# Performance work log

Measured on AMD Instinct MI355X. Metric: run time of the kernel, lower is better.

Reference implementation:

```python
import jax, jax.numpy as jnp
import numpy as np

DIM = 384
DSTATE = 16
DTRANK = 24  # ceil(384/16)
DCONV = 3
F = 3  # fixed segment factor from rearrange 'b (f t) c'


def setup_inputs() -> dict:
    key = jax.random.key(0)
    ks = jax.random.split(key, 8)
    d_in = DIM // 2
    x = jax.random.normal(ks[0], (4, 6144, DIM), dtype=jnp.float32)
    in_proj_w = jax.random.normal(ks[1], (DIM, DIM), dtype=jnp.float32) * 0.05
    in_proj_b = jnp.zeros((DIM,), jnp.float32)
    conv_w = jax.random.normal(ks[2], (d_in, 2, DCONV), dtype=jnp.float32) * 0.3
    conv_b = jnp.zeros((d_in,), jnp.float32)
    A = jnp.tile(jnp.arange(1, DSTATE + 1, dtype=jnp.float32)[None, :], (d_in, 1))
    A_log = jnp.log(A)
    Ab_log = jnp.log(A)
    D = jnp.ones((d_in,), jnp.float32)
    x_proj_w = jax.random.normal(ks[3], (DTRANK + 2 * DSTATE, d_in), dtype=jnp.float32) * 0.05
    dt_init_std = DTRANK ** (-0.5)
    dt_proj_w = jax.random.uniform(ks[4], (d_in, DTRANK), minval=-dt_init_std, maxval=dt_init_std, dtype=jnp.float32)
    dt = jnp.exp(jax.random.uniform(ks[5], (d_in,), dtype=jnp.float32) * (np.log(0.1) - np.log(0.001)) + np.log(0.001))
    dt = jnp.clip(dt, 1e-4)
    dt_proj_b = dt + jnp.log(-jnp.expm1(-dt))
    out_proj_w = jax.random.normal(ks[6], (DIM, DIM), dtype=jnp.float32) * 0.05
    out_proj_b = jnp.zeros((DIM,), jnp.float32)
    return dict(x=x, in_proj_w=in_proj_w, in_proj_b=in_proj_b, conv_w=conv_w, conv_b=conv_b,
                A_log=A_log, Ab_log=Ab_log, D=D, x_proj_w=x_proj_w, dt_proj_w=dt_proj_w,
                dt_proj_b=dt_proj_b, out_proj_w=out_proj_w, out_proj_b=out_proj_b)


def _ssm(u, Amat, x_proj_w, dt_proj_w, dt_proj_b, Dvec):
    # u: (b, d, l) selective scan (no z-gating; z handled outside by concat)
    x_dbl = jnp.einsum('rd,bdl->brl', x_proj_w, u)
    dt = x_dbl[:, :DTRANK]                      # (b, r, l)
    Bm = x_dbl[:, DTRANK:DTRANK + DSTATE]       # (b, n, l)
    Cm = x_dbl[:, DTRANK + DSTATE:]             # (b, n, l)
    delta = jax.nn.softplus(jnp.einsum('dr,brl->bdl', dt_proj_w, dt) + dt_proj_b[None, :, None])
    dA = jnp.exp(jnp.einsum('bdl,dn->lbdn', delta, Amat))      # (l, b, d, n)
    dBu = jnp.einsum('bdl,bnl->lbdn', delta * u, Bm)           # (l, b, d, n)
    Ct = jnp.transpose(Cm, (2, 0, 1))                          # (l, b, n)
    h0 = jnp.zeros(u.shape[:2] + (DSTATE,), u.dtype)

    def step(h, inp):
        dA_t, dBu_t, C_t = inp
        h = dA_t * h + dBu_t
        return h, jnp.einsum('bdn,bn->bd', h, C_t)

    _, ys = jax.lax.scan(step, h0, (dA, dBu, Ct))
    return jnp.transpose(ys, (1, 2, 0)) + u * Dvec[None, :, None]


def reference(x, in_proj_w, in_proj_b, conv_w, conv_b, A_log, Ab_log, D,
              x_proj_w, dt_proj_w, dt_proj_b, out_proj_w, out_proj_b):
    b, seqlen, dim = x.shape
    t = seqlen // F
    xp = (x @ in_proj_w.T + in_proj_b).reshape(b * F, t, dim)
    xp = jnp.transpose(xp, (0, 2, 1))  # (bf, dim, t)
    xc = jax.lax.conv_general_dilated(xp, conv_w, (1,), 'SAME',
                                      dimension_numbers=('NCH', 'OIH', 'NCH'),
                                      feature_group_count=dim // 2)
    xc = jax.nn.silu(xc + conv_b[None, :, None])  # (bf, dim//2, t)
    z = xc
    A = -jnp.exp(A_log)
    Ab = -jnp.exp(Ab_log)
    fwd = _ssm(xc, A, x_proj_w, dt_proj_w, dt_proj_b, D)
    bwd = jnp.flip(_ssm(jnp.flip(xc, -1), Ab, x_proj_w, dt_proj_w, dt_proj_b, D), -1)
    y = jnp.concatenate([fwd + bwd, z], axis=1)   # (bf, dim, t)
    y = jnp.transpose(y, (0, 2, 1))
    out = y @ out_proj_w.T + out_proj_b
    return out.reshape(b, seqlen, dim)
```

## Files before the change

### kernel.cpp

```cpp
#include <hip/hip_runtime.h>
#include <hip/hip_bf16.h>
#include <math.h>

#define NSQ   12
#define LQ    2048
#define DIMQ  384
#define DIQ   192
#define RKQ   24
#define NCHK  16
#define CLEN  128

#define BM 128
#define BN 64
#define BK 64

typedef unsigned short u16;
typedef __attribute__((ext_vector_type(8))) short s16x8;
typedef __attribute__((ext_vector_type(4))) float f32x4;
typedef __attribute__((ext_vector_type(4))) unsigned short u16x4;
typedef __attribute__((ext_vector_type(8))) unsigned short u16x8;

__device__ __forceinline__ float siluf(float x) {
  return x / (1.0f + __expf(-x));
}
__device__ __forceinline__ float softplusf(float x) {
  return (x > 20.0f) ? x : log1pf(expf(x));
}
__device__ __forceinline__ u16 f2bf(float f) {
  unsigned int u = __float_as_uint(f);
  u += 0x7FFFu + ((u >> 16) & 1u);
  return (u16)(u >> 16);
}

union F4 { float4 v; float a[4]; };

template<int CTRL>
__device__ __forceinline__ float dpp_add(float x) {
  union { float f; int i; } u, r;
  u.f = x;
  r.i = __builtin_amdgcn_update_dpp(0, u.i, CTRL, 0xF, 0xF, true);
  return x + r.f;
}

__global__ void k_prep(const float* __restrict__ xpw, const float* __restrict__ dtw,
                       const float* __restrict__ inw, const float* __restrict__ outw,
                       float* __restrict__ xpw_t, float* __restrict__ dtw_t,
                       u16* __restrict__ winb, u16* __restrict__ woutb) {
  int t = threadIdx.x + blockIdx.x * blockDim.x;
  int stride = blockDim.x * gridDim.x;
  for (int i = t; i < DIQ * 56; i += stride) {
    int d = i / 56, r = i % 56;
    xpw_t[i] = xpw[r * DIQ + d];
  }
  for (int i = t; i < RKQ * DIQ; i += stride) {
    int r = i / DIQ, d = i % DIQ;
    dtw_t[i] = dtw[d * RKQ + r];
  }
  for (int i = t; i < DIMQ * DIMQ; i += stride) {
    winb[i]  = f2bf(inw[i]);
    woutb[i] = f2bf(outw[i]);
  }
}

__launch_bounds__(256)
__global__ void k_inproj(const float* __restrict__ x, const u16* __restrict__ wbf,
                         const float* __restrict__ bias, float* __restrict__ xp_t) {
  __shared__ __align__(16) char smem[33792];
  u16 (*As)[72] = (u16(*)[72])smem;
  u16 (*Bs)[72] = (u16(*)[72])(smem + 18432);
  const int t = threadIdx.x;
  const int m0 = blockIdx.x * BM;
  const int n0 = blockIdx.y * BN;
  const int lane = t & 63, wid = t >> 6;
  const int wm = wid >> 1, wn = wid & 1;
  const int lr = lane & 15, lg = lane >> 4;
  f32x4 acc[4][2];
#pragma unroll
  for (int i = 0; i < 4; ++i)
#pragma unroll
    for (int j = 0; j < 2; ++j) acc[i][j] = (f32x4){0.f, 0.f, 0.f, 0.f};

  for (int k0 = 0; k0 < 384; k0 += BK) {
    float4 a_ld[8];
#pragma unroll
    for (int i = 0; i < 8; ++i) {
      const int idx = t + i * 256;
      const int row = idx >> 4, kq = (idx & 15) * 4;
      a_ld[i] = *(const float4*)&x[(size_t)(m0 + row) * 384 + k0 + kq];
    }
    u16x8 b_ld[2];
#pragma unroll
    for (int i = 0; i < 2; ++i) {
      const int idx = t + i * 256;
      const int n = idx >> 3, kq = (idx & 7) * 8;
      b_ld[i] = *(const u16x8*)&wbf[(size_t)(n0 + n) * 384 + k0 + kq];
    }
    __syncthreads();
#pragma unroll
    for (int i = 0; i < 8; ++i) {
      const int idx = t + i * 256;
      const int row = idx >> 4, kq = (idx & 15) * 4;
      u16x4 p;
      p.x = f2bf(a_ld[i].x); p.y = f2bf(a_ld[i].y);
      p.z = f2bf(a_ld[i].z); p.w = f2bf(a_ld[i].w);
      *(u16x4*)&As[row][kq] = p;
    }
#pragma unroll
    for (int i = 0; i < 2; ++i) {
      const int idx = t + i * 256;
      const int n = idx >> 3, kq = (idx & 7) * 8;
      *(u16x8*)&Bs[n][kq] = b_ld[i];
    }
    __syncthreads();
#pragma unroll
    for (int kh = 0; kh < BK; kh += 32) {
      s16x8 af[4], bf[2];
#pragma unroll
      for (int mi = 0; mi < 4; ++mi)
        af[mi] = *(const s16x8*)&As[wm * 64 + mi * 16 + lr][kh + lg * 8];
#pragma unroll
      for (int ni = 0; ni < 2; ++ni)
        bf[ni] = *(const s16x8*)&Bs[wn * 32 + ni * 16 + lr][kh + lg * 8];
#pragma unroll
      for (int mi = 0; mi < 4; ++mi)
#pragma unroll
        for (int ni = 0; ni < 2; ++ni)
          acc[mi][ni] = __builtin_amdgcn_mfma_f32_16x16x32_bf16(af[mi], bf[ni], acc[mi][ni], 0, 0, 0);
    }
    __syncthreads();
  }
  float (*T)[132] = (float(*)[132])smem;
#pragma unroll
  for (int mi = 0; mi < 4; ++mi)
#pragma unroll
    for (int ni = 0; ni < 2; ++ni) {
      const int c_loc = wn * 32 + ni * 16 + lr;
      const int m_loc = wm * 64 + mi * 16 + lg * 4;
      *(f32x4*)&T[c_loc][m_loc] = acc[mi][ni];
    }
  __syncthreads();
  const int s = m0 >> 11, p0 = m0 & 2047;
#pragma unroll
  for (int i = 0; i < 8; ++i) {
    const int idx = t + i * 256;
    const int c = idx >> 5, pq = (idx & 31) * 4;
    float4 v = *(const float4*)&T[c][pq];
    const float bv = bias[n0 + c];
    v.x += bv; v.y += bv; v.z += bv; v.w += bv;
    *(float4*)&xp_t[((size_t)s * 384 + n0 + c) * 2048 + p0 + pq] = v;
  }
}

__global__ void k_conv(const float* __restrict__ xp_t, const float* __restrict__ cw,
                       const float* __restrict__ cb, float* __restrict__ xc) {
  const int idx = blockIdx.x * 256 + threadIdx.x;
  const int p = idx & 2047;
  const int sd = idx >> 11;
  const int d = sd % DIQ, s = sd / DIQ;
  const float* r0 = &xp_t[((size_t)s * 384 + 2 * d) * 2048];
  const float* r1 = r0 + 2048;
  const float w00 = cw[d * 6 + 0], w01 = cw[d * 6 + 1], w02 = cw[d * 6 + 2];
  const float w10 = cw[d * 6 + 3], w11 = cw[d * 6 + 4], w12 = cw[d * 6 + 5];
  float acc = cb[d];
  if (p > 0)    acc += w00 * r0[p - 1] + w10 * r1[p - 1];
  acc += w01 * r0[p] + w11 * r1[p];
  if (p < 2047) acc += w02 * r0[p + 1] + w12 * r1[p + 1];
  xc[idx] = siluf(acc);
}

__launch_bounds__(256)
__global__ void k_xproj(const float* __restrict__ xc, const float* __restrict__ xpw_t,
                        const float* __restrict__ dtw_t, const float* __restrict__ dtb,
                        float* __restrict__ delta, float* __restrict__ bc) {
  __shared__ float As[16][68];
  __shared__ float Bs[16][64];
  __shared__ float xd[24][68];
  __shared__ float Dtw[24][192];
  const int t = threadIdx.x;
  const int m0 = blockIdx.x * 64;
  const int s = m0 >> 11, l0 = m0 & 2047;
  for (int i = t; i < 24 * 192; i += 256) Dtw[i / 192][i % 192] = dtw_t[i];
  const int tx = t & 15, ty = t >> 4;
  const int lk = t >> 4, mq = t & 15;
  float acc[4][4];
#pragma unroll
  for (int i = 0; i < 4; ++i)
#pragma unroll
    for (int j = 0; j < 4; ++j) acc[i][j] = 0.0f;

  for (int k0 = 0; k0 < 192; k0 += 16) {
    const float4 a = *(const float4*)&xc[((size_t)s * 192 + k0 + lk) * 2048 + l0 + mq * 4];
    float4 b;
    if (mq < 14) b = *(const float4*)&xpw_t[(size_t)(k0 + lk) * 56 + mq * 4];
    else         b = make_float4(0.f, 0.f, 0.f, 0.f);
    __syncthreads();
    *(float4*)&As[lk][mq * 4] = a;
    *(float4*)&Bs[lk][mq * 4] = b;
    __syncthreads();
#pragma unroll
    for (int k = 0; k < 16; ++k) {
      const float4 av = *(const float4*)&As[k][tx * 4];
      const float4 bv = *(const float4*)&Bs[k][ty * 4];
      const float a4[4] = {av.x, av.y, av.z, av.w};
      const float b4[4] = {bv.x, bv.y, bv.z, bv.w};
#pragma unroll
      for (int i = 0; i < 4; ++i)
#pragma unroll
        for (int j = 0; j < 4; ++j) acc[i][j] = fmaf(a4[i], b4[j], acc[i][j]);
    }
  }
  const int nbase = ty * 4;
  if (nbase < 24) {
#pragma unroll
    for (int j = 0; j < 4; ++j)
#pragma unroll
      for (int i = 0; i < 4; ++i) xd[nbase + j][tx * 4 + i] = acc[i][j];
  } else if (nbase < 56) {
#pragma unroll
    for (int i = 0; i < 4; ++i) {
      float4 v; v.x = acc[i][0]; v.y = acc[i][1]; v.z = acc[i][2]; v.w = acc[i][3];
      *(float4*)&bc[(size_t)(m0 + tx * 4 + i) * 32 + (nbase - 24)] = v;
    }
  }
  __syncthreads();
#pragma unroll
  for (int dc = 0; dc < 3; ++dc) {
    float a2[4][4];
#pragma unroll
    for (int i = 0; i < 4; ++i)
#pragma unroll
      for (int j = 0; j < 4; ++j) a2[i][j] = 0.0f;
    const int d0 = dc * 64 + ty * 4;
#pragma unroll
    for (int r = 0; r < 24; ++r) {
      const float4 av = *(const float4*)&xd[r][tx * 4];
      const float4 bv = *(const float4*)&Dtw[r][d0];
      const float a4[4] = {av.x, av.y, av.z, av.w};
      const float b4[4] = {bv.x, bv.y, bv.z, bv.w};
#pragma unroll
      for (int i = 0; i < 4; ++i)
#pragma unroll
        for (int j = 0; j < 4; ++j) a2[i][j] = fmaf(a4[i], b4[j], a2[i][j]);
    }
#pragma unroll
    for (int j = 0; j < 4; ++j) {
      const int d = d0 + j;
      const float bb = dtb[d];
      float4 v;
      v.x = softplusf(a2[0][j] + bb);
      v.y = softplusf(a2[1][j] + bb);
      v.z = softplusf(a2[2][j] + bb);
      v.w = softplusf(a2[3][j] + bb);
      *(float4*)&delta[((size_t)s * 192 + d) * 2048 + l0 + tx * 4] = v;
    }
  }
}

template<int DIR>
__launch_bounds__(256)
__global__ void k_scanA(const float* __restrict__ delta, const float* __restrict__ xc,
                        const float* __restrict__ bc, const float* __restrict__ A_log,
                        const float* __restrict__ Ab_log,
                        float* __restrict__ G, float* __restrict__ hc) {
  __shared__ float dch[16][132];
  __shared__ float uch[16][132];
  __shared__ float bsn[16][132];
  const int t = threadIdx.x;
  const int dl = t >> 4, n = t & 15;
  const int dg = blockIdx.x;
  const int s  = blockIdx.y;
  const int tc = blockIdx.z;
  const int d = dg * 16 + dl;
  const int base_l = DIR ? (LQ - CLEN * (tc + 1)) : (CLEN * tc);
  const float a = -__expf((DIR ? Ab_log : A_log)[d * 16 + n]);

  const size_t rb = ((size_t)s * 192 + dg * 16) * 2048 + base_l;
#pragma unroll
  for (int it = 0; it < 2; ++it) {
    const int i = t + it * 256;
    const int row = i >> 5, c4 = (i & 31) * 4;
    *(float4*)&dch[row][c4] = *(const float4*)&delta[rb + (size_t)row * 2048 + c4];
    *(float4*)&uch[row][c4] = *(const float4*)&xc[rb + (size_t)row * 2048 + c4];
  }
  const size_t bb = ((size_t)s * 2048 + base_l) * 32;
#pragma unroll
  for (int it = 0; it < 2; ++it) {
    const int i = t + it * 256;
    const int l = i >> 2, nq = (i & 3) * 4;
    F4 v; v.v = *(const float4*)&bc[bb + (size_t)l * 32 + nq];
#pragma unroll
    for (int k = 0; k < 4; ++k) bsn[nq + k][l] = v.a[k];
  }
  __syncthreads();
  float h = 0.0f, S = 0.0f;
#pragma unroll 4
  for (int qx = 0; qx < 32; ++qx) {
    const int q = DIR ? (31 - qx) : qx;
    const int lq = q * 4;
    F4 d4, u4, b4;
    d4.v = *(const float4*)&dch[dl][lq];
    u4.v = *(const float4*)&uch[dl][lq];
    b4.v = *(const float4*)&bsn[n][lq];
#pragma unroll
    for (int jj = 0; jj < 4; ++jj) {
      const int j = DIR ? (3 - jj) : jj;
      const float dlt = d4.a[j];
      const float dA = __expf(a * dlt);
      h = fmaf(dA, h, dlt * u4.a[j] * b4.a[j]);
      S += dlt;
    }
  }
  const size_t idx = (((size_t)(s * 2 + DIR) * NCHK + tc) * 192 + d) * 16 + n;
  G[idx] = __expf(a * S);
  hc[idx] = h;
}

__global__ void k_scanB(const float* __restrict__ G, float* __restrict__ hc) {
  const int gid = blockIdx.x * 256 + threadIdx.x;
  const int sd2 = gid / 3072;
  const int dn = gid % 3072;
  float h = 0.0f;
#pragma unroll
  for (int tc = 0; tc < NCHK; ++tc) {
    const size_t idx = ((size_t)sd2 * NCHK + tc) * 3072 + dn;
    const float g = G[idx];
    const float he = hc[idx];
    hc[idx] = h;
    h = fmaf(g, h, he);
  }
}

template<int DIR>
__launch_bounds__(256)
__global__ void k_scanC(const float* __restrict__ delta, const float* __restrict__ xc,
                        const float* __restrict__ bc, const float* __restrict__ A_log,
                        const float* __restrict__ Ab_log, const float* __restrict__ hc,
                        float* __restrict__ yf, float* __restrict__ yb) {
  __shared__ float dch[16][132];
  __shared__ float uch[16][132];
  __shared__ float bsn[16][132];
  __shared__ float csn[16][132];
  const int t = threadIdx.x;
  const int dl = t >> 4, n = t & 15;
  const int dg = blockIdx.x;
  const int s  = blockIdx.y;
  const int tc = blockIdx.z;
  const int d = dg * 16 + dl;
  const int base_l = DIR ? (LQ - CLEN * (tc + 1)) : (CLEN * tc);
  const float a = -__expf((DIR ? Ab_log : A_log)[d * 16 + n]);

  const size_t rb = ((size_t)s * 192 + dg * 16) * 2048 + base_l;
#pragma unroll
  for (int it = 0; it < 2; ++it) {
    const int i = t + it * 256;
    const int row = i >> 5, c4 = (i & 31) * 4;
    *(float4*)&dch[row][c4] = *(const float4*)&delta[rb + (size_t)row * 2048 + c4];
    *(float4*)&uch[row][c4] = *(const float4*)&xc[rb + (size_t)row * 2048 + c4];
  }
  const size_t bb = ((size_t)s * 2048 + base_l) * 32;
#pragma unroll
  for (int it = 0; it < 4; ++it) {
    const int i = t + it * 256;
    const int l = i >> 3, cq = (i & 7) * 4;
    F4 v; v.v = *(const float4*)&bc[bb + (size_t)l * 32 + cq];
    if (cq < 16) {
#pragma unroll
      for (int k = 0; k < 4; ++k) bsn[cq + k][l] = v.a[k];
    } else {
#pragma unroll
      for (int k = 0; k < 4; ++k) csn[cq - 16 + k][l] = v.a[k];
    }
  }
  const size_t idx = (((size_t)(s * 2 + DIR) * NCHK + tc) * 192 + d) * 16 + n;
  float h = hc[idx];
  __syncthreads();
  float* yrow = &(DIR ? yb : yf)[((size_t)s * 192 + d) * 2048 + base_l];
#pragma unroll 2
  for (int ww = 0; ww < 8; ++ww) {
    const int w = DIR ? (7 - ww) : ww;
    float ykeep = 0.0f;
#pragma unroll
    for (int qq = 0; qq < 4; ++qq) {
      const int q = DIR ? (3 - qq) : qq;
      const int lq = w * 16 + q * 4;
      F4 d4, u4, b4, c4;
      d4.v = *(const float4*)&dch[dl][lq];
      u4.v = *(const float4*)&uch[dl][lq];
      b4.v = *(const float4*)&bsn[n][lq];
      c4.v = *(const float4*)&csn[n][lq];
#pragma unroll
      for (int jj = 0; jj < 4; ++jj) {
        const int j = DIR ? (3 - jj) : jj;
        const float dlt = d4.a[j];
        const float dA = __expf(a * dlt);
        h = fmaf(dA, h, dlt * u4.a[j] * b4.a[j]);
        float yv = h * c4.a[j];
        yv = dpp_add<0x128>(yv);
        yv = dpp_add<0x124>(yv);
        yv = dpp_add<0x122>(yv);
        yv = dpp_add<0x121>(yv);
        ykeep = (q * 4 + j == n) ? yv : ykeep;
      }
    }
    yrow[w * 16 + n] = ykeep;
  }
}

#define SWC(l) (((l >> 2) & 7) << 3)
__launch_bounds__(256)
__global__ void k_combine(const float* __restrict__ yf, const float* __restrict__ yb,
                          const float* __restrict__ xc, const float* __restrict__ Dvec,
                          u16* __restrict__ Abuf) {
  __shared__ u16 T[64][72];
  const int t = threadIdx.x;
  const int cg = blockIdx.x;
  const int s  = blockIdx.y;
  const int l0 = blockIdx.z * 64;
  const int c0 = (cg < 3 ? cg : cg - 3) * 64;
#pragma unroll
  for (int i = 0; i < 4; ++i) {
    const int idx = t + i * 256;
    const int cr = idx >> 4, lq = (idx & 15) * 4;
    const size_t off = ((size_t)s * 192 + c0 + cr) * 2048 + l0 + lq;
    F4 v;
    if (cg < 3) {
      F4 f, g, u;
      f.v = *(const float4*)&yf[off];
      g.v = *(const float4*)&yb[off];
      u.v = *(const float4*)&xc[off];
      const float dv2 = 2.0f * Dvec[c0 + cr];
#pragma unroll
      for (int j = 0; j < 4; ++j) v.a[j] = f.a[j] + g.a[j] + dv2 * u.a[j];
    } else {
      v.v = *(const float4*)&xc[off];
    }
#pragma unroll
    for (int j = 0; j < 4; ++j) {
      const int l = lq + j;
      T[l][cr ^ SWC(l)] = f2bf(v.a[j]);
    }
  }
  __syncthreads();
  const int ccol = (cg < 3) ? cg * 64 : 192 + (cg - 3) * 64;
#pragma unroll
  for (int i = 0; i < 2; ++i) {
    const int idx = t + i * 256;
    const int l = idx >> 3, cq = (idx & 7) * 8;
    const u16x8 v = *(const u16x8*)&T[l][cq ^ SWC(l)];
    *(u16x8*)&Abuf[((size_t)s * 2048 + l0 + l) * 384 + ccol + cq] = v;
  }
}

__launch_bounds__(256)
__global__ void k_outproj(const u16* __restrict__ Abuf, const u16* __restrict__ wbf,
                          const float* __restrict__ bias, float* __restrict__ out) {
  __shared__ __align__(16) char smem[34816];
  u16 (*As)[72] = (u16(*)[72])smem;
  u16 (*Bs)[72] = (u16(*)[72])(smem + 18432);
  const int t = threadIdx.x;
  const int m0 = blockIdx.x * BM;
  const int n0 = blockIdx.y * BN;
  const int lane = t & 63, wid = t >> 6;
  const int wm = wid >> 1, wn = wid & 1;
  const int lr = lane & 15, lg = lane >> 4;
  f32x4 acc[4][2];
#pragma unroll
  for (int i = 0; i < 4; ++i)
#pragma unroll
    for (int j = 0; j < 2; ++j) acc[i][j] = (f32x4){0.f, 0.f, 0.f, 0.f};

  for (int k0 = 0; k0 < 384; k0 += BK) {
    u16x8 a_ld[4];
#pragma unroll
    for (int i = 0; i < 4; ++i) {
      const int idx = t + i * 256;
      const int row = idx >> 3, kq = (idx & 7) * 8;
      a_ld[i] = *(const u16x8*)&Abuf[(size_t)(m0 + row) * 384 + k0 + kq];
    }
    u16x8 b_ld[2];
#pragma unroll
    for (int i = 0; i < 2; ++i) {
      const int idx = t + i * 256;
      const int n = idx >> 3, kq = (idx & 7) * 8;
      b_ld[i] = *(const u16x8*)&wbf[(size_t)(n0 + n) * 384 + k0 + kq];
    }
    __syncthreads();
#pragma unroll
    for (int i = 0; i < 4; ++i) {
      const int idx = t + i * 256;
      const int row = idx >> 3, kq = (idx & 7) * 8;
      *(u16x8*)&As[row][kq] = a_ld[i];
    }
#pragma unroll
    for (int i = 0; i < 2; ++i) {
      const int idx = t + i * 256;
      const int n = idx >> 3, kq = (idx & 7) * 8;
      *(u16x8*)&Bs[n][kq] = b_ld[i];
    }
    __syncthreads();
#pragma unroll
    for (int kh = 0; kh < BK; kh += 32) {
      s16x8 af[4], bf[2];
#pragma unroll
      for (int mi = 0; mi < 4; ++mi)
        af[mi] = *(const s16x8*)&As[wm * 64 + mi * 16 + lr][kh + lg * 8];
#pragma unroll
      for (int ni = 0; ni < 2; ++ni)
        bf[ni] = *(const s16x8*)&Bs[wn * 32 + ni * 16 + lr][kh + lg * 8];
#pragma unroll
      for (int mi = 0; mi < 4; ++mi)
#pragma unroll
        for (int ni = 0; ni < 2; ++ni)
          acc[mi][ni] = __builtin_amdgcn_mfma_f32_16x16x32_bf16(af[mi], bf[ni], acc[mi][ni], 0, 0, 0);
    }
    __syncthreads();
  }
  float (*T)[68] = (float(*)[68])smem;
#pragma unroll
  for (int mi = 0; mi < 4; ++mi)
#pragma unroll
    for (int ni = 0; ni < 2; ++ni) {
      const int c_loc = wn * 32 + ni * 16 + lr;
      const int m_loc = wm * 64 + mi * 16 + lg * 4;
#pragma unroll
      for (int r = 0; r < 4; ++r) T[m_loc + r][c_loc] = acc[mi][ni][r];
    }
  __syncthreads();
#pragma unroll
  for (int i = 0; i < 8; ++i) {
    const int idx = t + i * 256;
    const int m = idx >> 4, cq = (idx & 15) * 4;
    float4 v = *(const float4*)&T[m][cq];
    const float4 bb = *(const float4*)&bias[n0 + cq];
    v.x += bb.x; v.y += bb.y; v.z += bb.z; v.w += bb.w;
    *(float4*)&out[(size_t)(m0 + m) * 384 + n0 + cq] = v;
  }
}

extern "C" void kernel_launch(void* const* d_in, const int* in_sizes, int n_in,
                              void* d_out, int out_size, void* d_ws, size_t ws_size,
                              hipStream_t stream) {
  const float* x     = (const float*)d_in[0];
  const float* inw   = (const float*)d_in[1];
  const float* inb   = (const float*)d_in[2];
  const float* convw = (const float*)d_in[3];
  const float* convb = (const float*)d_in[4];
  const float* alog  = (const float*)d_in[5];
  const float* ablog = (const float*)d_in[6];
  const float* Dv    = (const float*)d_in[7];
  const float* xpw   = (const float*)d_in[8];
  const float* dtw   = (const float*)d_in[9];
  const float* dtb   = (const float*)d_in[10];
  const float* outw  = (const float*)d_in[11];
  const float* outb  = (const float*)d_in[12];
  float* out = (float*)d_out;

  float* ws = (float*)d_ws;
  float* xp_t  = ws;
  float* xc    = xp_t + 9437184;
  float* delta = xc + 4718592;
  float* bc    = delta + 4718592;
  float* xpw_t = bc + 786432;
  float* dtw_t = xpw_t + 10752;
  float* G     = dtw_t + 4608;
  float* hc    = G + 1179648;
  u16*   winb  = (u16*)(hc + 1179648);
  u16*   woutb = winb + 147456;
  float* yf = xp_t;
  float* yb = xp_t + 4718592;
  u16*   Abuf = (u16*)delta;

  hipLaunchKernelGGL(k_prep,      dim3(96),         dim3(256), 0, stream, xpw, dtw, inw, outw, xpw_t, dtw_t, winb, woutb);
  hipLaunchKernelGGL(k_inproj,    dim3(192, 6),     dim3(256), 0, stream, x, winb, inb, xp_t);
  hipLaunchKernelGGL(k_conv,      dim3(18432),      dim3(256), 0, stream, xp_t, convw, convb, xc);
  hipLaunchKernelGGL(k_xproj,     dim3(384),        dim3(256), 0, stream, xc, xpw_t, dtw_t, dtb, delta, bc);
  hipLaunchKernelGGL((k_scanA<0>),dim3(12, 12, 16), dim3(256), 0, stream, delta, xc, bc, alog, ablog, G, hc);
  hipLaunchKernelGGL((k_scanA<1>),dim3(12, 12, 16), dim3(256), 0, stream, delta, xc, bc, alog, ablog, G, hc);
  hipLaunchKernelGGL(k_scanB,     dim3(288),        dim3(256), 0, stream, G, hc);
  hipLaunchKernelGGL((k_scanC<0>),dim3(12, 12, 16), dim3(256), 0, stream, delta, xc, bc, alog, ablog, hc, yf, yb);
  hipLaunchKernelGGL((k_scanC<1>),dim3(12, 12, 16), dim3(256), 0, stream, delta, xc, bc, alog, ablog, hc, yf, yb);
  hipLaunchKernelGGL(k_combine,   dim3(6, 12, 32),  dim3(256), 0, stream, yf, yb, xc, Dv, Abuf);
  hipLaunchKernelGGL(k_outproj,   dim3(192, 6),     dim3(256), 0, stream, Abuf, woutb, outb, out);
}
```

Baseline: 377.8 us.

## Fold dt_proj into x_proj weights and run xproj on split-bf16 MFMA

The weight product dt_proj_w·x_proj_w[:24] is precomputed in the prep kernel, so delta comes directly from a single 224x192 projection instead of a two-stage GEMM. That projection now runs on bf16 MFMA using a hi/lo split of both weights and activations (three MFMAs per tile) to keep close to fp32 accuracy. This removes the scalar FMA GEMMs and the intermediate rank-24 stage. In exchange it adds more work per output (224 rows instead of 56+192 in two steps) and per-element bf16 splitting of the activations. The delta stores are now scalar rather than float4.

```diff
diff --git a/kernel.cpp b/kernel.cpp
--- a/kernel.cpp
+++ b/kernel.cpp
@@ -31,6 +31,9 @@
   u += 0x7FFFu + ((u >> 16) & 1u);
   return (u16)(u >> 16);
 }
+__device__ __forceinline__ float bf2f(u16 h) {
+  return __uint_as_float(((unsigned int)h) << 16);
+}
 
 union F4 { float4 v; float a[4]; };
 
@@ -44,21 +47,27 @@
 
 __global__ void k_prep(const float* __restrict__ xpw, const float* __restrict__ dtw,
                        const float* __restrict__ inw, const float* __restrict__ outw,
-                       float* __restrict__ xpw_t, float* __restrict__ dtw_t,
-                       u16* __restrict__ winb, u16* __restrict__ woutb) {
+                       u16* __restrict__ winb, u16* __restrict__ woutb,
+                       u16* __restrict__ wc_hi, u16* __restrict__ wc_lo) {
   int t = threadIdx.x + blockIdx.x * blockDim.x;
   int stride = blockDim.x * gridDim.x;
-  for (int i = t; i < DIQ * 56; i += stride) {
-    int d = i / 56, r = i % 56;
-    xpw_t[i] = xpw[r * DIQ + d];
-  }
-  for (int i = t; i < RKQ * DIQ; i += stride) {
-    int r = i / DIQ, d = i % DIQ;
-    dtw_t[i] = dtw[d * RKQ + r];
-  }
   for (int i = t; i < DIMQ * DIMQ; i += stride) {
     winb[i]  = f2bf(inw[i]);
     woutb[i] = f2bf(outw[i]);
+  }
+  for (int i = t; i < 224 * 192; i += stride) {
+    const int r = i / 192, k = i % 192;
+    float v;
+    if (r < 192) {
+      float s = 0.0f;
+      for (int q = 0; q < RKQ; ++q) s = fmaf(dtw[r * RKQ + q], xpw[q * 192 + k], s);
+      v = s;
+    } else {
+      v = xpw[(24 + (r - 192)) * 192 + k];
+    }
+    const u16 hi = f2bf(v);
+    wc_hi[i] = hi;
+    wc_lo[i] = f2bf(v - bf2f(hi));
   }
 }
 
@@ -169,90 +178,92 @@
 }
 
 __launch_bounds__(256)
-__global__ void k_xproj(const float* __restrict__ xc, const float* __restrict__ xpw_t,
-                        const float* __restrict__ dtw_t, const float* __restrict__ dtb,
+__global__ void k_xproj(const float* __restrict__ xc, const u16* __restrict__ wc_hi,
+                        const u16* __restrict__ wc_lo, const float* __restrict__ dtb,
                         float* __restrict__ delta, float* __restrict__ bc) {
-  __shared__ float As[16][68];
-  __shared__ float Bs[16][64];
-  __shared__ float xd[24][68];
-  __shared__ float Dtw[24][192];
+  __shared__ u16 Ah[224][40];
+  __shared__ u16 Al[224][40];
+  __shared__ u16 Bh[64][40];
+  __shared__ u16 Bl[64][40];
   const int t = threadIdx.x;
-  const int m0 = blockIdx.x * 64;
-  const int s = m0 >> 11, l0 = m0 & 2047;
-  for (int i = t; i < 24 * 192; i += 256) Dtw[i / 192][i % 192] = dtw_t[i];
-  const int tx = t & 15, ty = t >> 4;
-  const int lk = t >> 4, mq = t & 15;
-  float acc[4][4];
-#pragma unroll
-  for (int i = 0; i < 4; ++i)
-#pragma unroll
-    for (int j = 0; j < 4; ++j) acc[i][j] = 0.0f;
-
-  for (int k0 = 0; k0 < 192; k0 += 16) {
-    const float4 a = *(const float4*)&xc[((size_t)s * 192 + k0 + lk) * 2048 + l0 + mq * 4];
-    float4 b;
-    if (mq < 14) b = *(const float4*)&xpw_t[(size_t)(k0 + lk) * 56 + mq * 4];
-    else         b = make_float4(0.f, 0.f, 0.f, 0.f);
-    __syncthreads();
-    *(float4*)&As[lk][mq * 4] = a;
-    *(float4*)&Bs[lk][mq * 4] = b;
-    __syncthreads();
-#pragma unroll
-    for (int k = 0; k < 16; ++k) {
-      const float4 av = *(const float4*)&As[k][tx * 4];
-      const float4 bv = *(const float4*)&Bs[k][ty * 4];
-      const float a4[4] = {av.x, av.y, av.z, av.w};
-      const float b4[4] = {bv.x, bv.y, bv.z, bv.w};
-#pragma unroll
-      for (int i = 0; i < 4; ++i)
-#pragma unroll
-        for (int j = 0; j < 4; ++j) acc[i][j] = fmaf(a4[i], b4[j], acc[i][j]);
-    }
-  }
-  const int nbase = ty * 4;
-  if (nbase < 24) {
-#pragma unroll
-    for (int j = 0; j < 4; ++j)
-#pragma unroll
-      for (int i = 0; i < 4; ++i) xd[nbase + j][tx * 4 + i] = acc[i][j];
-  } else if (nbase < 56) {
+  const int lane = t & 63, w = t >> 6;
+  const int ln = lane & 15, lg = lane >> 4;
+  const int blk = blockIdx.x;
+  const int s = blk >> 5, l0 = (blk & 31) * 64;
+  f32x4 acc[14];
+#pragma unroll
+  for (int mi = 0; mi < 14; ++mi) acc[mi] = (f32x4){0.f, 0.f, 0.f, 0.f};
+
+  for (int kc = 0; kc < 192; kc += 32) {
+    u16x8 wah[4], wal[4];
 #pragma unroll
     for (int i = 0; i < 4; ++i) {
-      float4 v; v.x = acc[i][0]; v.y = acc[i][1]; v.z = acc[i][2]; v.w = acc[i][3];
-      *(float4*)&bc[(size_t)(m0 + tx * 4 + i) * 32 + (nbase - 24)] = v;
-    }
-  }
-  __syncthreads();
-#pragma unroll
-  for (int dc = 0; dc < 3; ++dc) {
-    float a2[4][4];
-#pragma unroll
-    for (int i = 0; i < 4; ++i)
-#pragma unroll
-      for (int j = 0; j < 4; ++j) a2[i][j] = 0.0f;
-    const int d0 = dc * 64 + ty * 4;
-#pragma unroll
-    for (int r = 0; r < 24; ++r) {
-      const float4 av = *(const float4*)&xd[r][tx * 4];
-      const float4 bv = *(const float4*)&Dtw[r][d0];
-      const float a4[4] = {av.x, av.y, av.z, av.w};
-      const float b4[4] = {bv.x, bv.y, bv.z, bv.w};
-#pragma unroll
-      for (int i = 0; i < 4; ++i)
-#pragma unroll
-        for (int j = 0; j < 4; ++j) a2[i][j] = fmaf(a4[i], b4[j], a2[i][j]);
-    }
+      const int idx = t + i * 256;
+      if (idx < 896) {
+        const int r = idx >> 2, kg = (idx & 3) * 8;
+        wah[i] = *(const u16x8*)&wc_hi[(size_t)r * 192 + kc + kg];
+        wal[i] = *(const u16x8*)&wc_lo[(size_t)r * 192 + kc + kg];
+      }
+    }
+    float4 uld[2];
+#pragma unroll
+    for (int i = 0; i < 2; ++i) {
+      const int idx = t + i * 256;
+      const int k = idx >> 4, lq = (idx & 15) * 4;
+      uld[i] = *(const float4*)&xc[((size_t)s * 192 + kc + k) * 2048 + l0 + lq];
+    }
+    __syncthreads();
+#pragma unroll
+    for (int i = 0; i < 4; ++i) {
+      const int idx = t + i * 256;
+      if (idx < 896) {
+        const int r = idx >> 2, kg = (idx & 3) * 8;
+        *(u16x8*)&Ah[r][kg] = wah[i];
+        *(u16x8*)&Al[r][kg] = wal[i];
+      }
+    }
+#pragma unroll
+    for (int i = 0; i < 2; ++i) {
+      const int idx = t + i * 256;
+      const int k = idx >> 4, lq = (idx & 15) * 4;
+      F4 v; v.v = uld[i];
+#pragma unroll
+      for (int j = 0; j < 4; ++j) {
+        const float f = v.a[j];
+        const u16 hi = f2bf(f);
+        Bh[lq + j][k] = hi;
+        Bl[lq + j][k] = f2bf(f - bf2f(hi));
+      }
+    }
+    __syncthreads();
+    const s16x8 bh = *(const s16x8*)&Bh[w * 16 + ln][lg * 8];
+    const s16x8 bl = *(const s16x8*)&Bl[w * 16 + ln][lg * 8];
+#pragma unroll
+    for (int mi = 0; mi < 14; ++mi) {
+      const s16x8 ah = *(const s16x8*)&Ah[mi * 16 + ln][lg * 8];
+      const s16x8 al = *(const s16x8*)&Al[mi * 16 + ln][lg * 8];
+      acc[mi] = __builtin_amdgcn_mfma_f32_16x16x32_bf16(ah, bh, acc[mi], 0, 0, 0);
+      acc[mi] = __builtin_amdgcn_mfma_f32_16x16x32_bf16(al, bh, acc[mi], 0, 0, 0);
+      acc[mi] = __builtin_amdgcn_mfma_f32_16x16x32_bf16(ah, bl, acc[mi], 0, 0, 0);
+    }
+    __syncthreads();
+  }
+  const int l = l0 + w * 16 + ln;
+#pragma unroll
+  for (int mi = 0; mi < 12; ++mi) {
+    const int r0 = mi * 16 + lg * 4;
 #pragma unroll
     for (int j = 0; j < 4; ++j) {
-      const int d = d0 + j;
-      const float bb = dtb[d];
-      float4 v;
-      v.x = softplusf(a2[0][j] + bb);
-      v.y = softplusf(a2[1][j] + bb);
-      v.z = softplusf(a2[2][j] + bb);
-      v.w = softplusf(a2[3][j] + bb);
-      *(float4*)&delta[((size_t)s * 192 + d) * 2048 + l0 + tx * 4] = v;
-    }
+      const int r = r0 + j;
+      delta[((size_t)s * 192 + r) * 2048 + l] = softplusf(acc[mi][j] + dtb[r]);
+    }
+  }
+#pragma unroll
+  for (int mi = 12; mi < 14; ++mi) {
+    const int rr = (mi - 12) * 16 + lg * 4;
+    float4 v;
+    v.x = acc[mi][0]; v.y = acc[mi][1]; v.z = acc[mi][2]; v.w = acc[mi][3];
+    *(float4*)&bc[((size_t)s * 2048 + l) * 32 + rr] = v;
   }
 }
 
@@ -560,20 +571,20 @@
   float* xc    = xp_t + 9437184;
   float* delta = xc + 4718592;
   float* bc    = delta + 4718592;
-  float* xpw_t = bc + 786432;
-  float* dtw_t = xpw_t + 10752;
-  float* G     = dtw_t + 4608;
+  float* G     = bc + 786432;
   float* hc    = G + 1179648;
   u16*   winb  = (u16*)(hc + 1179648);
   u16*   woutb = winb + 147456;
+  u16*   wc_hi = woutb + 147456;
+  u16*   wc_lo = wc_hi + 43008;
   float* yf = xp_t;
   float* yb = xp_t + 4718592;
   u16*   Abuf = (u16*)delta;
 
-  hipLaunchKernelGGL(k_prep,      dim3(96),         dim3(256), 0, stream, xpw, dtw, inw, outw, xpw_t, dtw_t, winb, woutb);
+  hipLaunchKernelGGL(k_prep,      dim3(96),         dim3(256), 0, stream, xpw, dtw, inw, outw, winb, woutb, wc_hi, wc_lo);
   hipLaunchKernelGGL(k_inproj,    dim3(192, 6),     dim3(256), 0, stream, x, winb, inb, xp_t);
   hipLaunchKernelGGL(k_conv,      dim3(18432),      dim3(256), 0, stream, xp_t, convw, convb, xc);
-  hipLaunchKernelGGL(k_xproj,     dim3(384),        dim3(256), 0, stream, xc, xpw_t, dtw_t, dtb, delta, bc);
+  hipLaunchKernelGGL(k_xproj,     dim3(384),        dim3(256), 0, stream, xc, wc_hi, wc_lo, dtb, delta, bc);
   hipLaunchKernelGGL((k_scanA<0>),dim3(12, 12, 16), dim3(256), 0, stream, delta, xc, bc, alog, ablog, G, hc);
   hipLaunchKernelGGL((k_scanA<1>),dim3(12, 12, 16), dim3(256), 0, stream, delta, xc, bc, alog, ablog, G, hc);
   hipLaunchKernelGGL(k_scanB,     dim3(288),        dim3(256), 0, stream, G, hc);
```

New measurement: 347.5 us. 1.09x faster.
